# Kernel optimization log

Hardware: AMD Instinct MI355X
Metric: run time of the kernel (lower is better)

The kernel has to match this reference:

```python
import jax, jax.numpy as jnp
import numpy as np

N_USERS = 100000
N_ENTITY = 100000
D = 64
N_RK = 3
B = 16384
LA = 20   # authors per user
LC = 5    # genres per user


def setup_inputs() -> dict:
    key = jax.random.key(0)
    ks = jax.random.split(key, 6)
    return {
        "user_id": jax.random.randint(ks[0], (B,), 0, N_USERS),
        "artists_id": jax.random.randint(ks[1], (B, LA), 0, N_ENTITY),
        "categories_id": jax.random.randint(ks[2], (B, LC), 0, N_ENTITY),
        "rate": 0,  # dropout prob; eval mode -> identity
        "user_factors": jax.random.normal(ks[3], (N_USERS, D), jnp.float32),
        "entity_factors": jax.random.normal(ks[4], (N_ENTITY, D), jnp.float32),
        "relation_k": jax.random.normal(ks[5], (D, N_RK), jnp.float32),
    }


def _contrib(idx, users, entity_factors):
    # idx: [B, L] entity indices; users: [B, D]
    emb = entity_factors[idx]                      # [B, L, D] gather
    pre = jnp.einsum("bld,bd->bl", emb, users)     # per-aspect mat-vec (niubi)
    return pre.mean(axis=1), pre                   # mean over segment -> [B]


def reference(user_id, artists_id, categories_id, rate, user_factors,
              entity_factors, relation_k):
    users = user_factors[user_id]                               # [B, D]
    # importance of each aspect type
    scores = jax.nn.softmax(
        jax.nn.leaky_relu(users @ relation_k, negative_slope=0.2), axis=1)  # [B, 3]
    s_act = scores[:, 0]
    s_dir = scores[:, 1]
    # contribution of each aspect (ragged gather-matvec-mean, vectorized)
    c_act, niubi_act = _contrib(artists_id, users, entity_factors)
    c_dir, niubi_dir = _contrib(categories_id, users, entity_factors)
    importance_sum = s_act + s_dir
    prediction = (c_act * s_act + c_dir * s_dir) / importance_sum
    return prediction, scores, c_act, c_dir, niubi_act, niubi_dir
```

## Files before the change

kernel.cpp:

```cpp
#include <hip/hip_runtime.h>

constexpr int B  = 16384;
constexpr int D  = 64;
constexpr int LA = 20;
constexpr int LC = 5;

template <int CTRL>
__device__ __forceinline__ float ror_add(float v) {
    const int r = __builtin_amdgcn_update_dpp(
        0, __float_as_int(v), CTRL, 0xF, 0xF, true);
    return v + __int_as_float(r);
}

template <int N>
__device__ __forceinline__ void reduce16(float (&p)[N]) {
    #pragma unroll
    for (int l = 0; l < N; ++l) p[l] = ror_add<0x128>(p[l]);
    #pragma unroll
    for (int l = 0; l < N; ++l) p[l] = ror_add<0x124>(p[l]);
    #pragma unroll
    for (int l = 0; l < N; ++l) p[l] = ror_add<0x122>(p[l]);
    #pragma unroll
    for (int l = 0; l < N; ++l) p[l] = ror_add<0x121>(p[l]);
}

__global__ __launch_bounds__(256, 4) void aspect_kernel(
    const int*   __restrict__ user_id,
    const int*   __restrict__ artists_id,
    const int*   __restrict__ categories_id,
    const float* __restrict__ user_factors,
    const float* __restrict__ entity_factors,
    const float* __restrict__ relation_k,
    float*       __restrict__ out)
{
    const int tid = threadIdx.x;
    const int sl  = tid & 15;
    const int grp = tid >> 4;
    const int b   = (blockIdx.x << 4) + grp;

    float* pred    = out;
    float* scores  = out + B;
    float* c_act_o = out + (size_t)4 * B;
    float* c_dir_o = out + (size_t)5 * B;
    float* niubiA  = out + (size_t)6 * B;
    float* niubiC  = niubiA + (size_t)B * LA;

    const int    uid = user_id[b];
    const float4 u4  = *(const float4*)&user_factors[(size_t)uid * D + sl * 4];

    float ps[3];
    {
        const int d0 = sl * 4;
        ps[0] = fmaf(u4.x, relation_k[(d0+0)*3+0], fmaf(u4.y, relation_k[(d0+1)*3+0],
                fmaf(u4.z, relation_k[(d0+2)*3+0], u4.w * relation_k[(d0+3)*3+0])));
        ps[1] = fmaf(u4.x, relation_k[(d0+0)*3+1], fmaf(u4.y, relation_k[(d0+1)*3+1],
                fmaf(u4.z, relation_k[(d0+2)*3+1], u4.w * relation_k[(d0+3)*3+1])));
        ps[2] = fmaf(u4.x, relation_k[(d0+0)*3+2], fmaf(u4.y, relation_k[(d0+1)*3+2],
                fmaf(u4.z, relation_k[(d0+2)*3+2], u4.w * relation_k[(d0+3)*3+2])));
    }
    reduce16(ps);
    float q0 = ps[0] >= 0.f ? ps[0] : 0.2f * ps[0];
    float q1 = ps[1] >= 0.f ? ps[1] : 0.2f * ps[1];
    float q2 = ps[2] >= 0.f ? ps[2] : 0.2f * ps[2];
    const float m   = fmaxf(q0, fmaxf(q1, q2));
    const float e0  = __expf(q0 - m), e1 = __expf(q1 - m), e2 = __expf(q2 - m);
    const float inv = 1.f / (e0 + e1 + e2);
    const float s0 = e0 * inv, s1 = e1 * inv, s2 = e2 * inv;

    float pa[LA];
    #pragma unroll
    for (int l = 0; l < LA; ++l) {
        const int    idx = artists_id[b * LA + l];
        const float4 e   = *(const float4*)&entity_factors[(size_t)idx * D + sl * 4];
        pa[l] = fmaf(e.x, u4.x, fmaf(e.y, u4.y, fmaf(e.z, u4.z, e.w * u4.w)));
    }
    reduce16(pa);
    float sumA = 0.f;
    #pragma unroll
    for (int l = 0; l < LA; ++l) sumA += pa[l];
    const float c_act = sumA * (1.f / LA);

    float pc[LC];
    #pragma unroll
    for (int l = 0; l < LC; ++l) {
        const int    idx = categories_id[b * LC + l];
        const float4 e   = *(const float4*)&entity_factors[(size_t)idx * D + sl * 4];
        pc[l] = fmaf(e.x, u4.x, fmaf(e.y, u4.y, fmaf(e.z, u4.z, e.w * u4.w)));
    }
    reduce16(pc);
    float sumC = 0.f;
    #pragma unroll
    for (int l = 0; l < LC; ++l) sumC += pc[l];
    const float c_dir = sumC * (1.f / LC);

    if (sl < 5) {
        float4 v;
        v.x = sl == 0 ? pa[0] : sl == 1 ? pa[4]  : sl == 2 ? pa[8]  : sl == 3 ? pa[12] : pa[16];
        v.y = sl == 0 ? pa[1] : sl == 1 ? pa[5]  : sl == 2 ? pa[9]  : sl == 3 ? pa[13] : pa[17];
        v.z = sl == 0 ? pa[2] : sl == 1 ? pa[6]  : sl == 2 ? pa[10] : sl == 3 ? pa[14] : pa[18];
        v.w = sl == 0 ? pa[3] : sl == 1 ? pa[7]  : sl == 2 ? pa[11] : sl == 3 ? pa[15] : pa[19];
        *(float4*)&niubiA[(size_t)b * LA + sl * 4] = v;
    }
    if (sl < LC) {
        const float v = sl == 0 ? pc[0] : sl == 1 ? pc[1] : sl == 2 ? pc[2] : sl == 3 ? pc[3] : pc[4];
        niubiC[(size_t)b * LC + sl] = v;
    }
    if (sl < 3) {
        const float v = sl == 0 ? s0 : sl == 1 ? s1 : s2;
        scores[b * 3 + sl] = v;
    }
    if (sl == 0) {
        pred[b]    = (c_act * s0 + c_dir * s1) / (s0 + s1);
        c_act_o[b] = c_act;
        c_dir_o[b] = c_dir;
    }
}

extern "C" void kernel_launch(void* const* d_in, const int* in_sizes, int n_in,
                              void* d_out, int out_size, void* d_ws, size_t ws_size,
                              hipStream_t stream) {
    const int*   user_id        = (const int*)d_in[0];
    const int*   artists_id     = (const int*)d_in[1];
    const int*   categories_id  = (const int*)d_in[2];
    const float* user_factors   = (const float*)d_in[4];
    const float* entity_factors = (const float*)d_in[5];
    const float* relation_k     = (const float*)d_in[6];
    float*       out            = (float*)d_out;

    const int rows_per_block = 16;
    const int grid = B / rows_per_block;
    aspect_kernel<<<grid, 256, 0, stream>>>(
        user_id, artists_id, categories_id, user_factors, entity_factors, relation_k, out);
}
```

Before: 104.4 us.

## Split each row's gathers across two wavefronts with shared-memory combine

Each batch row is now handled by two wavefronts. One gathers and reduces the first 16 artist embeddings. The other handles the remaining 4 artists, the 5 categories and the softmax scores. The first half's partial sum goes through shared memory, and a block-wide barrier precedes the final prediction write. The aim is to double the number of wavefronts issuing gathers and to cut per-thread register pressure, adding latency hiding for this memory-bound gather. In exchange it adds a __syncthreads and a 16-vs-9 load imbalance between the two halves.

```diff
diff --git a/kernel.cpp b/kernel.cpp
--- a/kernel.cpp
+++ b/kernel.cpp
@@ -4,6 +4,7 @@
 constexpr int D  = 64;
 constexpr int LA = 20;
 constexpr int LC = 5;
+constexpr int SPLIT = 16;
 
 template <int CTRL>
 __device__ __forceinline__ float ror_add(float v) {
@@ -24,7 +25,7 @@
     for (int l = 0; l < N; ++l) p[l] = ror_add<0x121>(p[l]);
 }
 
-__global__ __launch_bounds__(256, 4) void aspect_kernel(
+__global__ __launch_bounds__(512, 8) void aspect_kernel(
     const int*   __restrict__ user_id,
     const int*   __restrict__ artists_id,
     const int*   __restrict__ categories_id,
@@ -33,10 +34,16 @@
     const float* __restrict__ relation_k,
     float*       __restrict__ out)
 {
-    const int tid = threadIdx.x;
-    const int sl  = tid & 15;
-    const int grp = tid >> 4;
-    const int b   = (blockIdx.x << 4) + grp;
+    const int tid  = threadIdx.x;
+    const int lane = tid & 63;
+    const int sl   = lane & 15;
+    const int grp  = lane >> 4;
+    const int wid  = tid >> 6;
+    const int half = wid & 1;
+    const int rowInBlk = (wid >> 1) * 4 + grp;
+    const int b = (blockIdx.x << 4) + rowInBlk;
+
+    __shared__ float s_partA[16];
 
     float* pred    = out;
     float* scores  = out + B;
@@ -48,68 +55,91 @@
     const int    uid = user_id[b];
     const float4 u4  = *(const float4*)&user_factors[(size_t)uid * D + sl * 4];
 
-    float ps[3];
-    {
-        const int d0 = sl * 4;
-        ps[0] = fmaf(u4.x, relation_k[(d0+0)*3+0], fmaf(u4.y, relation_k[(d0+1)*3+0],
-                fmaf(u4.z, relation_k[(d0+2)*3+0], u4.w * relation_k[(d0+3)*3+0])));
-        ps[1] = fmaf(u4.x, relation_k[(d0+0)*3+1], fmaf(u4.y, relation_k[(d0+1)*3+1],
-                fmaf(u4.z, relation_k[(d0+2)*3+1], u4.w * relation_k[(d0+3)*3+1])));
-        ps[2] = fmaf(u4.x, relation_k[(d0+0)*3+2], fmaf(u4.y, relation_k[(d0+1)*3+2],
-                fmaf(u4.z, relation_k[(d0+2)*3+2], u4.w * relation_k[(d0+3)*3+2])));
+    float sumB = 0.f, sumC = 0.f, s0 = 0.f, s1 = 0.f, s2 = 0.f;
+
+    if (half == 0) {
+        float pa[SPLIT];
+        #pragma unroll
+        for (int l = 0; l < SPLIT; ++l) {
+            const int    idx = artists_id[b * LA + l];
+            const float4 e   = *(const float4*)&entity_factors[(size_t)idx * D + sl * 4];
+            pa[l] = fmaf(e.x, u4.x, fmaf(e.y, u4.y, fmaf(e.z, u4.z, e.w * u4.w)));
+        }
+        reduce16(pa);
+        if (sl < 4) {
+            float4 v;
+            v.x = sl == 0 ? pa[0] : sl == 1 ? pa[4] : sl == 2 ? pa[8]  : pa[12];
+            v.y = sl == 0 ? pa[1] : sl == 1 ? pa[5] : sl == 2 ? pa[9]  : pa[13];
+            v.z = sl == 0 ? pa[2] : sl == 1 ? pa[6] : sl == 2 ? pa[10] : pa[14];
+            v.w = sl == 0 ? pa[3] : sl == 1 ? pa[7] : sl == 2 ? pa[11] : pa[15];
+            *(float4*)&niubiA[(size_t)b * LA + sl * 4] = v;
+        }
+        float part = 0.f;
+        #pragma unroll
+        for (int l = 0; l < SPLIT; ++l) part += pa[l];
+        if (sl == 0) s_partA[rowInBlk] = part;
+    } else {
+        float pa[LA - SPLIT];
+        #pragma unroll
+        for (int l = 0; l < LA - SPLIT; ++l) {
+            const int    idx = artists_id[b * LA + SPLIT + l];
+            const float4 e   = *(const float4*)&entity_factors[(size_t)idx * D + sl * 4];
+            pa[l] = fmaf(e.x, u4.x, fmaf(e.y, u4.y, fmaf(e.z, u4.z, e.w * u4.w)));
+        }
+        float pc[LC];
+        #pragma unroll
+        for (int l = 0; l < LC; ++l) {
+            const int    idx = categories_id[b * LC + l];
+            const float4 e   = *(const float4*)&entity_factors[(size_t)idx * D + sl * 4];
+            pc[l] = fmaf(e.x, u4.x, fmaf(e.y, u4.y, fmaf(e.z, u4.z, e.w * u4.w)));
+        }
+
+        float ps[3];
+        {
+            const int d0 = sl * 4;
+            ps[0] = fmaf(u4.x, relation_k[(d0+0)*3+0], fmaf(u4.y, relation_k[(d0+1)*3+0],
+                    fmaf(u4.z, relation_k[(d0+2)*3+0], u4.w * relation_k[(d0+3)*3+0])));
+            ps[1] = fmaf(u4.x, relation_k[(d0+0)*3+1], fmaf(u4.y, relation_k[(d0+1)*3+1],
+                    fmaf(u4.z, relation_k[(d0+2)*3+1], u4.w * relation_k[(d0+3)*3+1])));
+            ps[2] = fmaf(u4.x, relation_k[(d0+0)*3+2], fmaf(u4.y, relation_k[(d0+1)*3+2],
+                    fmaf(u4.z, relation_k[(d0+2)*3+2], u4.w * relation_k[(d0+3)*3+2])));
+        }
+        reduce16(ps);
+        const float q0 = ps[0] >= 0.f ? ps[0] : 0.2f * ps[0];
+        const float q1 = ps[1] >= 0.f ? ps[1] : 0.2f * ps[1];
+        const float q2 = ps[2] >= 0.f ? ps[2] : 0.2f * ps[2];
+        const float m   = fmaxf(q0, fmaxf(q1, q2));
+        const float e0  = __expf(q0 - m), e1 = __expf(q1 - m), e2 = __expf(q2 - m);
+        const float inv = 1.f / (e0 + e1 + e2);
+        s0 = e0 * inv; s1 = e1 * inv; s2 = e2 * inv;
+
+        reduce16(pa);
+        reduce16(pc);
+
+        if (sl == 0) {
+            float4 v; v.x = pa[0]; v.y = pa[1]; v.z = pa[2]; v.w = pa[3];
+            *(float4*)&niubiA[(size_t)b * LA + SPLIT] = v;
+        }
+        if (sl < LC) {
+            const float v = sl == 0 ? pc[0] : sl == 1 ? pc[1] : sl == 2 ? pc[2] : sl == 3 ? pc[3] : pc[4];
+            niubiC[(size_t)b * LC + sl] = v;
+        }
+        if (sl < 3) {
+            const float v = sl == 0 ? s0 : sl == 1 ? s1 : s2;
+            scores[b * 3 + sl] = v;
+        }
+        #pragma unroll
+        for (int l = 0; l < LA - SPLIT; ++l) sumB += pa[l];
+        #pragma unroll
+        for (int l = 0; l < LC; ++l) sumC += pc[l];
     }
-    reduce16(ps);
-    float q0 = ps[0] >= 0.f ? ps[0] : 0.2f * ps[0];
-    float q1 = ps[1] >= 0.f ? ps[1] : 0.2f * ps[1];
-    float q2 = ps[2] >= 0.f ? ps[2] : 0.2f * ps[2];
-    const float m   = fmaxf(q0, fmaxf(q1, q2));
-    const float e0  = __expf(q0 - m), e1 = __expf(q1 - m), e2 = __expf(q2 - m);
-    const float inv = 1.f / (e0 + e1 + e2);
-    const float s0 = e0 * inv, s1 = e1 * inv, s2 = e2 * inv;
 
-    float pa[LA];
-    #pragma unroll
-    for (int l = 0; l < LA; ++l) {
-        const int    idx = artists_id[b * LA + l];
-        const float4 e   = *(const float4*)&entity_factors[(size_t)idx * D + sl * 4];
-        pa[l] = fmaf(e.x, u4.x, fmaf(e.y, u4.y, fmaf(e.z, u4.z, e.w * u4.w)));
-    }
-    reduce16(pa);
-    float sumA = 0.f;
-    #pragma unroll
-    for (int l = 0; l < LA; ++l) sumA += pa[l];
-    const float c_act = sumA * (1.f / LA);
+    __syncthreads();
 
-    float pc[LC];
-    #pragma unroll
-    for (int l = 0; l < LC; ++l) {
-        const int    idx = categories_id[b * LC + l];
-        const float4 e   = *(const float4*)&entity_factors[(size_t)idx * D + sl * 4];
-        pc[l] = fmaf(e.x, u4.x, fmaf(e.y, u4.y, fmaf(e.z, u4.z, e.w * u4.w)));
-    }
-    reduce16(pc);
-    float sumC = 0.f;
-    #pragma unroll
-    for (int l = 0; l < LC; ++l) sumC += pc[l];
-    const float c_dir = sumC * (1.f / LC);
-
-    if (sl < 5) {
-        float4 v;
-        v.x = sl == 0 ? pa[0] : sl == 1 ? pa[4]  : sl == 2 ? pa[8]  : sl == 3 ? pa[12] : pa[16];
-        v.y = sl == 0 ? pa[1] : sl == 1 ? pa[5]  : sl == 2 ? pa[9]  : sl == 3 ? pa[13] : pa[17];
-        v.z = sl == 0 ? pa[2] : sl == 1 ? pa[6]  : sl == 2 ? pa[10] : sl == 3 ? pa[14] : pa[18];
-        v.w = sl == 0 ? pa[3] : sl == 1 ? pa[7]  : sl == 2 ? pa[11] : sl == 3 ? pa[15] : pa[19];
-        *(float4*)&niubiA[(size_t)b * LA + sl * 4] = v;
-    }
-    if (sl < LC) {
-        const float v = sl == 0 ? pc[0] : sl == 1 ? pc[1] : sl == 2 ? pc[2] : sl == 3 ? pc[3] : pc[4];
-        niubiC[(size_t)b * LC + sl] = v;
-    }
-    if (sl < 3) {
-        const float v = sl == 0 ? s0 : sl == 1 ? s1 : s2;
-        scores[b * 3 + sl] = v;
-    }
-    if (sl == 0) {
+    if (half == 1 && sl == 0) {
+        const float sumA  = s_partA[rowInBlk] + sumB;
+        const float c_act = sumA * (1.f / LA);
+        const float c_dir = sumC * (1.f / LC);
         pred[b]    = (c_act * s0 + c_dir * s1) / (s0 + s1);
         c_act_o[b] = c_act;
         c_dir_o[b] = c_dir;
@@ -129,6 +159,6 @@
 
     const int rows_per_block = 16;
     const int grid = B / rows_per_block;
-    aspect_kernel<<<grid, 256, 0, stream>>>(
+    aspect_kernel<<<grid, 512, 0, stream>>>(
         user_id, artists_id, categories_id, user_factors, entity_factors, relation_k, out);
 }
```

Result: slower. 109.6 us (+5.0%).
